# Performance work log

Measured on AMD Instinct MI355X. Metric: run time of the kernel, lower is better.

Reference implementation:

```python
import jax, jax.numpy as jnp
import numpy as np

BN_EPS = 1e-3
SLOPE = 0.1
K = 100
CLUSTER_TEMP = 5.0


def setup_inputs() -> dict:
    key = jax.random.key(0)
    ks = jax.random.split(key, 5)
    N, Cin, Cout = 8192, 1, 64
    d = 49 * Cout  # (28/4)^2 * out_channels
    return {
        "x": jax.random.normal(ks[0], (N, Cin, 28, 28), jnp.float32),
        "conv1_w": jax.random.normal(ks[1], (128, Cin, 5, 5), jnp.float32) * 0.05,
        "conv1_b": jnp.zeros((128,), jnp.float32),
        "bn1_gamma": jnp.ones((128,), jnp.float32),
        "bn1_beta": jnp.zeros((128,), jnp.float32),
        "bn1_mean": jnp.zeros((128,), jnp.float32),
        "bn1_var": jnp.ones((128,), jnp.float32),
        "conv2_w": jax.random.normal(ks[2], (Cout, 128, 5, 5), jnp.float32) * 0.02,
        "conv2_b": jnp.zeros((Cout,), jnp.float32),
        "bn2_gamma": jnp.ones((Cout,), jnp.float32),
        "bn2_beta": jnp.zeros((Cout,), jnp.float32),
        "bn2_mean": jnp.zeros((Cout,), jnp.float32),
        "bn2_var": jnp.ones((Cout,), jnp.float32),
        "init_mu": jax.random.uniform(ks[3], (K, d), jnp.float32),
        "num_iter": 10,
    }


def _conv_bn_lrelu(x, w, b, gamma, beta, mean, var):
    # Conv2d(k=5, s=2, p=2) -> BatchNorm (eval/running stats) -> LeakyReLU(0.1)
    h = jax.lax.conv_general_dilated(
        x, w, window_strides=(2, 2), padding=[(2, 2), (2, 2)],
        dimension_numbers=("NCHW", "OIHW", "NCHW"))
    h = h + b[None, :, None, None]
    inv = gamma * jax.lax.rsqrt(var + BN_EPS)
    h = h * inv[None, :, None, None] + (beta - mean * inv)[None, :, None, None]
    return jnp.where(h >= 0, h, SLOPE * h)


def _cluster(data, mu, num_iter):
    # Row L2-normalize (equivalent to diag(1/||row||) @ data)
    data = data / jnp.linalg.norm(data, axis=1, keepdims=True)  # [n, d]
    for _ in range(num_iter):
        dist = data @ mu.T                                 # [n, K]
        r = jax.nn.softmax(CLUSTER_TEMP * dist, axis=1)    # [n, K]
        cluster_r = r.sum(axis=0)                          # [K]
        cluster_mean = r.T @ data                          # [K, d]
        mu = cluster_mean / cluster_r[:, None]
    dist = data @ mu.T
    r = jax.nn.softmax(CLUSTER_TEMP * dist, axis=1)
    return mu, r, dist


def reference(x, conv1_w, conv1_b, bn1_gamma, bn1_beta, bn1_mean, bn1_var,
              conv2_w, conv2_b, bn2_gamma, bn2_beta, bn2_mean, bn2_var,
              init_mu, num_iter):
    h = _conv_bn_lrelu(x, conv1_w, conv1_b, bn1_gamma, bn1_beta, bn1_mean, bn1_var)
    h = _conv_bn_lrelu(h, conv2_w, conv2_b, bn2_gamma, bn2_beta, bn2_mean, bn2_var)
    embeds = h.reshape(h.shape[0], -1)                     # [N, 49*Cout]
    mu_init, _, _ = _cluster(embeds, init_mu, int(num_iter))
    mu, r, dist = _cluster(embeds, jax.lax.stop_gradient(mu_init), 1)
    return mu, r, dist
```

## Files before the change

kernel.cpp:

```cpp
#include <hip/hip_runtime.h>
#include <hip/hip_bf16.h>
#include <math.h>

#define BN_EPS 1e-3f
#define SLOPE  0.1f
#define TEMP   5.0f
#define DDIM   3136

typedef __attribute__((ext_vector_type(8))) short bf16x8;
typedef __attribute__((ext_vector_type(4))) float f32x4;

static __device__ __forceinline__ short f2b(float f) {
  __hip_bfloat16 h = __float2bfloat16(f);
  return *reinterpret_cast<short*>(&h);
}

#define W2B_OFF   0u
#define W1B_OFF   102400u
#define DB_OFF    204800u
#define DB_SZ     (8192u*3136u/2u)
#define DT_OFF    (DB_OFF + DB_SZ)
#define DT_SZ     (8192u*3136u/2u)
#define MUB_OFF   (DT_OFF + DT_SZ)
#define MUB_SZ    (112u*3136u/2u)
#define MUF_OFF   (MUB_OFF + MUB_SZ)
#define MUF_SZ    (100u*3136u)
#define CMS_OFF   (MUF_OFF + MUF_SZ)
#define CMS_SZ    (8u*3136u*112u)
#define RT_OFF    (CMS_OFF + CMS_SZ)
#define RT_SZ     (112u*8192u/2u)
#define CR_OFF    (RT_OFF + RT_SZ)

__global__ __launch_bounds__(256) void k_w2b(const float* __restrict__ w2,
                                             __hip_bfloat16* __restrict__ w2b) {
  int idx = blockIdx.x * 256 + threadIdx.x;
  if (idx >= 204800) return;
  int ci   = idx & 31;
  int lr   = (idx >> 5) & 15;
  int rest = idx >> 9;
  int kk   = rest % 100;
  int oct  = rest / 100;
  int oc   = oct * 16 + lr;
  int tap  = kk >> 2;
  int c    = ((kk & 3) << 5) + ci;
  w2b[idx] = __float2bfloat16(w2[(oc * 128 + c) * 25 + tap]);
}

__global__ __launch_bounds__(256) void k_w1b(const float* __restrict__ w1,
                                             __hip_bfloat16* __restrict__ w1b) {
  int idx = blockIdx.x * 256 + threadIdx.x;
  if (idx >= 4096) return;
  int k   = idx & 31;
  int lr  = (idx >> 5) & 15;
  int oct = idx >> 9;
  int oc  = oct * 16 + lr;
  float v = (k < 25) ? w1[oc * 25 + k] : 0.f;
  w1b[idx] = __float2bfloat16(v);
}

__global__ __launch_bounds__(256) void k_conv(
    const float* __restrict__ x,
    const __hip_bfloat16* __restrict__ w1bh, const float* __restrict__ b1,
    const float* __restrict__ g1,  const float* __restrict__ be1,
    const float* __restrict__ mn1, const float* __restrict__ vr1,
    const __hip_bfloat16* __restrict__ w2bh, const float* __restrict__ b2,
    const float* __restrict__ g2,  const float* __restrict__ be2,
    const float* __restrict__ mn2, const float* __restrict__ vr2,
    __hip_bfloat16* __restrict__ db) {
  __shared__ float xs[1024];
  __shared__ float bn2s[128];
  __shared__ float bn1a[128], bn1b[128];
  __shared__ float nrm[4];
  __shared__ __align__(16) __hip_bfloat16 h1s[197 * 128];

  const int t    = threadIdx.x;
  const int img  = blockIdx.x;
  const int lane = t & 63;
  const int wv   = t >> 6;
  const int lr   = lane & 15;
  const int kg   = lane >> 4;
  const short* w2b = (const short*)w2bh;
  const short* w1b = (const short*)w1bh;

  for (int i = t; i < 1024; i += 256) xs[i] = 0.f;
  if (t < 64) {
    float a2 = g2[t] * rsqrtf(vr2[t] + BN_EPS);
    bn2s[t]      = a2;
    bn2s[64 + t] = b2[t] * a2 + be2[t] - mn2[t] * a2;
    ((unsigned*)(h1s + 196 * 128))[t] = 0u;
  }
  if (t < 128) {
    float a1 = g1[t] * rsqrtf(vr1[t] + BN_EPS);
    bn1a[t] = a1;
    bn1b[t] = b1[t] * a1 + be1[t] - mn1[t] * a1;
  }
  __syncthreads();
  const float* xi = x + (size_t)img * 784;
  for (int i = t; i < 784; i += 256) {
    int yy = i / 28, xx = i % 28;
    xs[(yy + 2) * 32 + (xx + 2)] = xi[i];
  }
  __syncthreads();

  {
    bf16x8 a0 = *(const bf16x8*)(w1b + (2 * wv) * 512 + lr * 32 + kg * 8);
    bf16x8 a1 = *(const bf16x8*)(w1b + (2 * wv + 1) * 512 + lr * 32 + kg * 8);
    for (int pt = 0; pt < 13; ++pt) {
      const int px  = pt * 16 + lr;
      const int pxc = (px < 196) ? px : 195;
      const int oy  = pxc / 14, ox = pxc - 14 * (pxc / 14);
      const float* xb = xs + (2 * oy) * 32 + 2 * ox;
      short bs[8];
#pragma unroll
      for (int j = 0; j < 8; ++j) {
        int k   = kg * 8 + j;
        int tap = (k < 25) ? k : 0;
        int kh  = tap / 5, kw = tap - 5 * (tap / 5);
        bs[j] = f2b(xb[kh * 32 + kw]);
      }
      bf16x8 b;
#pragma unroll
      for (int j = 0; j < 8; ++j) b[j] = bs[j];
      f32x4 c0 = {0.f, 0.f, 0.f, 0.f}, c1 = {0.f, 0.f, 0.f, 0.f};
      c0 = __builtin_amdgcn_mfma_f32_16x16x32_bf16(a0, b, c0, 0, 0, 0);
      c1 = __builtin_amdgcn_mfma_f32_16x16x32_bf16(a1, b, c1, 0, 0, 0);
      if (px < 196) {
        const int swz = (px & 7) << 4;
        unsigned w0lo, w0hi, w1lo, w1hi;
        {
          float v[4], u[4];
#pragma unroll
          for (int r = 0; r < 4; ++r) {
            int oc = wv * 32 + kg * 4 + r;
            float h = c0[r] * bn1a[oc] + bn1b[oc];
            v[r] = (h >= 0.f) ? h : SLOPE * h;
            int oc2 = oc + 16;
            float h2 = c1[r] * bn1a[oc2] + bn1b[oc2];
            u[r] = (h2 >= 0.f) ? h2 : SLOPE * h2;
          }
          w0lo = (unsigned)(unsigned short)f2b(v[0]) |
                 ((unsigned)(unsigned short)f2b(v[1]) << 16);
          w0hi = (unsigned)(unsigned short)f2b(v[2]) |
                 ((unsigned)(unsigned short)f2b(v[3]) << 16);
          w1lo = (unsigned)(unsigned short)f2b(u[0]) |
                 ((unsigned)(unsigned short)f2b(u[1]) << 16);
          w1hi = (unsigned)(unsigned short)f2b(u[2]) |
                 ((unsigned)(unsigned short)f2b(u[3]) << 16);
        }
        char* base = (char*)h1s + px * 256;
        const int o0 = ((wv * 32 + kg * 4) * 2) ^ swz;
        const int o1 = ((wv * 32 + 16 + kg * 4) * 2) ^ swz;
        *(uint2*)(base + o0) = make_uint2(w0lo, w0hi);
        *(uint2*)(base + o1) = make_uint2(w1lo, w1hi);
      }
    }
  }
  __syncthreads();

  const int woff  = lr * 32 + kg * 8;
  const int kgoff = kg << 4;
  int pxA[4], oyA[4], oxA[4];
#pragma unroll
  for (int pt = 0; pt < 4; ++pt) {
    int p = pt * 16 + lr;
    pxA[pt] = p;
    oyA[pt] = p / 7;
    oxA[pt] = p - 7 * oyA[pt];
  }

  f32x4 acc[4][4];
#pragma unroll
  for (int oct = 0; oct < 4; ++oct)
#pragma unroll
    for (int pt = 0; pt < 4; ++pt) acc[oct][pt] = (f32x4){0.f, 0.f, 0.f, 0.f};

  const int s0 = 25 * wv, s1e = s0 + 25;
  int curtap = -1;
  int rowB[4], rowS[4];

  auto loadk = [&](int kk, bf16x8* areg, bf16x8* breg) {
    int tap = kk >> 2;
    if (tap != curtap) {
      curtap = tap;
      int kh = tap / 5, kw = tap - 5 * (tap / 5);
#pragma unroll
      for (int pt = 0; pt < 4; ++pt) {
        int iy = 2 * oyA[pt] - 2 + kh;
        int ix = 2 * oxA[pt] - 2 + kw;
        bool val = (pxA[pt] < 49) & ((unsigned)iy < 14u) & ((unsigned)ix < 14u);
        int ip = val ? iy * 14 + ix : 196;
        rowB[pt] = ip * 256;
        rowS[pt] = (ip & 7) << 4;
      }
    }
    int c01 = (kk & 3) << 6;
#pragma unroll
    for (int oct = 0; oct < 4; ++oct)
      areg[oct] = *(const bf16x8*)(w2b + ((oct * 100 + kk) << 9) + woff);
#pragma unroll
    for (int pt = 0; pt < 4; ++pt)
      breg[pt] = *(const bf16x8*)((const char*)h1s + rowB[pt] +
                                  ((c01 | kgoff) ^ rowS[pt]));
  };

  bf16x8 a[4], b[4], an[4], bn_[4];
  loadk(s0, a, b);
  for (int kk = s0; kk < s1e; ++kk) {
    if (kk + 1 < s1e) loadk(kk + 1, an, bn_);
#pragma unroll
    for (int oct = 0; oct < 4; ++oct)
#pragma unroll
      for (int pt = 0; pt < 4; ++pt)
        acc[oct][pt] = __builtin_amdgcn_mfma_f32_16x16x32_bf16(a[oct], b[pt],
                                                               acc[oct][pt], 0, 0, 0);
#pragma unroll
    for (int q = 0; q < 4; ++q) { a[q] = an[q]; b[q] = bn_[q]; }
  }
  __syncthreads();

  float* red = (float*)h1s;
  if (wv != 0) {
#pragma unroll
    for (int oct = 0; oct < 4; ++oct)
#pragma unroll
      for (int pt = 0; pt < 4; ++pt)
#pragma unroll
        for (int r = 0; r < 4; ++r)
          red[(wv - 1) * 4096 + ((oct * 4 + pt) * 4 + r) * 64 + lane] =
              acc[oct][pt][r];
  }
  __syncthreads();
  if (wv == 0) {
#pragma unroll
    for (int oct = 0; oct < 4; ++oct)
#pragma unroll
      for (int pt = 0; pt < 4; ++pt)
#pragma unroll
        for (int r = 0; r < 4; ++r) {
          const int i = (oct * 4 + pt) * 4 + r;
          float v = acc[oct][pt][r] + red[i * 64 + lane] +
                    red[4096 + i * 64 + lane] + red[8192 + i * 64 + lane];
          red[i * 64 + lane] = v;
        }
  }
  __syncthreads();

  float outv[16];
  float ss = 0.f;
#pragma unroll
  for (int pt = 0; pt < 4; ++pt) {
#pragma unroll
    for (int r = 0; r < 4; ++r) {
      const int i = ((wv * 4 + pt) * 4 + r);
      float v = red[i * 64 + lane];
      const int oc = wv * 16 + kg * 4 + r;
      v = v * bn2s[oc] + bn2s[64 + oc];
      v = (v >= 0.f) ? v : SLOPE * v;
      outv[pt * 4 + r] = v;
      if (pxA[pt] < 49) ss += v * v;
    }
  }
#pragma unroll
  for (int m = 1; m < 64; m <<= 1) ss += __shfl_xor(ss, m, 64);
  if (lane == 0) nrm[wv] = ss;
  __syncthreads();
  const float invn = rsqrtf(nrm[0] + nrm[1] + nrm[2] + nrm[3]);
  __hip_bfloat16* dro = db + (size_t)img * DDIM;
#pragma unroll
  for (int pt = 0; pt < 4; ++pt) {
    if (pxA[pt] < 49) {
#pragma unroll
      for (int r = 0; r < 4; ++r) {
        const int oc = wv * 16 + kg * 4 + r;
        dro[oc * 49 + pxA[pt]] = __float2bfloat16(outv[pt * 4 + r] * invn);
      }
    }
  }
}

__global__ __launch_bounds__(256) void k_tr(const __hip_bfloat16* __restrict__ dbh,
                                            __hip_bfloat16* __restrict__ dTh) {
  __shared__ short tile[64][72];
  const int t   = threadIdx.x;
  const int i   = t >> 2;
  const int seg = t & 3;
  const size_t img0 = (size_t)blockIdx.x * 64;
  const size_t d0   = (size_t)blockIdx.y * 64;
  const short* src = (const short*)dbh + (img0 + i) * DDIM + d0 + seg * 16;
  bf16x8 v0 = *(const bf16x8*)src;
  bf16x8 v1 = *(const bf16x8*)(src + 8);
  *(bf16x8*)&tile[i][seg * 16]     = v0;
  *(bf16x8*)&tile[i][seg * 16 + 8] = v1;
  __syncthreads();
  short tmp[16];
#pragma unroll
  for (int k = 0; k < 16; ++k) tmp[k] = tile[seg * 16 + k][i];
  short* dst = (short*)dTh + (d0 + i) * 8192 + img0 + seg * 16;
  *(bf16x8*)dst       = *(bf16x8*)tmp;
  *(bf16x8*)(dst + 8) = *((bf16x8*)tmp + 1);
}

__global__ __launch_bounds__(256) void k_muinit(const float* __restrict__ mu0,
                                                __hip_bfloat16* __restrict__ mub) {
  int idx = blockIdx.x * 256 + threadIdx.x;
  if (idx >= 112 * DDIM) return;
  int j = idx / DDIM, d = idx - j * DDIM;
  float v = (j < 100) ? mu0[j * DDIM + d] : 0.f;
  mub[idx] = __float2bfloat16(v);
}

__global__ __launch_bounds__(256) void k_dsm(
    const __hip_bfloat16* __restrict__ data,
    const __hip_bfloat16* __restrict__ mu,
    __hip_bfloat16* __restrict__ rT,
    float* __restrict__ cr,
    float* __restrict__ outr,
    float* __restrict__ outd,
    int final_flag) {
  __shared__ float red[3][64][28];
  const int t    = threadIdx.x;
  const int lane = t & 63;
  const int wv   = t >> 6;
  const int rowbase = blockIdx.x * 16;
  const int s0 = (98 * wv) >> 2;
  const int s1 = (98 * (wv + 1)) >> 2;
  const int lr = lane & 15;
  const int kg = lane >> 4;

  const __hip_bfloat16* arow = data + (size_t)(rowbase + lr) * DDIM + kg * 8;
  const __hip_bfloat16* brow = mu + (size_t)lr * DDIM + kg * 8;

  f32x4 acc[7];
#pragma unroll
  for (int i = 0; i < 7; ++i) acc[i] = (f32x4){0.f, 0.f, 0.f, 0.f};

  bf16x8 a, b[7], an, bn_[7];
  {
    const int k0 = s0 * 32;
    a = *(const bf16x8*)(arow + k0);
#pragma unroll
    for (int tl = 0; tl < 7; ++tl)
      b[tl] = *(const bf16x8*)(brow + (size_t)tl * 16 * DDIM + k0);
  }
  for (int s = s0; s < s1; ++s) {
    if (s + 1 < s1) {
      const int k1 = (s + 1) * 32;
      an = *(const bf16x8*)(arow + k1);
#pragma unroll
      for (int tl = 0; tl < 7; ++tl)
        bn_[tl] = *(const bf16x8*)(brow + (size_t)tl * 16 * DDIM + k1);
    }
#pragma unroll
    for (int tl = 0; tl < 7; ++tl)
      acc[tl] = __builtin_amdgcn_mfma_f32_16x16x32_bf16(a, b[tl], acc[tl], 0, 0, 0);
    a = an;
#pragma unroll
    for (int tl = 0; tl < 7; ++tl) b[tl] = bn_[tl];
  }

  if (wv != 0) {
#pragma unroll
    for (int tl = 0; tl < 7; ++tl)
#pragma unroll
      for (int r = 0; r < 4; ++r) red[wv - 1][lane][tl * 4 + r] = acc[tl][r];
  }
  __syncthreads();
  if (wv != 0) return;

#pragma unroll
  for (int tl = 0; tl < 7; ++tl)
#pragma unroll
    for (int r = 0; r < 4; ++r)
      acc[tl][r] += red[0][lane][tl * 4 + r] + red[1][lane][tl * 4 + r] +
                    red[2][lane][tl * 4 + r];

  if (final_flag) {
#pragma unroll
    for (int tl = 0; tl < 7; ++tl) {
      const int col = tl * 16 + lr;
      if (col < 100) {
#pragma unroll
        for (int r = 0; r < 4; ++r)
          outd[(size_t)(rowbase + kg * 4 + r) * 100 + col] = acc[tl][r];
      }
    }
  }

#pragma unroll
  for (int r = 0; r < 4; ++r) {
    float m = -1e30f;
#pragma unroll
    for (int tl = 0; tl < 7; ++tl) {
      const bool valid = (tl < 6) || (lr < 4);
      m = fmaxf(m, valid ? acc[tl][r] : -1e30f);
    }
    m = fmaxf(m, __shfl_xor(m, 1, 64));
    m = fmaxf(m, __shfl_xor(m, 2, 64));
    m = fmaxf(m, __shfl_xor(m, 4, 64));
    m = fmaxf(m, __shfl_xor(m, 8, 64));
    float s = 0.f;
    float e[7];
#pragma unroll
    for (int tl = 0; tl < 7; ++tl) {
      const bool valid = (tl < 6) || (lr < 4);
      e[tl] = valid ? __expf(TEMP * (acc[tl][r] - m)) : 0.f;
      s += e[tl];
    }
    s += __shfl_xor(s, 1, 64);
    s += __shfl_xor(s, 2, 64);
    s += __shfl_xor(s, 4, 64);
    s += __shfl_xor(s, 8, 64);
    const float inv = 1.f / s;
#pragma unroll
    for (int tl = 0; tl < 7; ++tl) acc[tl][r] = e[tl] * inv;
  }

  if (final_flag) {
#pragma unroll
    for (int tl = 0; tl < 7; ++tl) {
      const int col = tl * 16 + lr;
      if (col < 100) {
#pragma unroll
        for (int r = 0; r < 4; ++r)
          outr[(size_t)(rowbase + kg * 4 + r) * 100 + col] = acc[tl][r];
      }
    }
    return;
  }

#pragma unroll
  for (int tl = 0; tl < 7; ++tl) {
    const int col = tl * 16 + lr;
    if (col < 100) {
#pragma unroll
      for (int r = 0; r < 4; ++r)
        rT[(size_t)col * 8192 + rowbase + kg * 4 + r] = __float2bfloat16(acc[tl][r]);
    }
  }
  float csum[7];
#pragma unroll
  for (int tl = 0; tl < 7; ++tl) {
    float cs = acc[tl][0] + acc[tl][1] + acc[tl][2] + acc[tl][3];
    cs += __shfl_xor(cs, 16, 64);
    cs += __shfl_xor(cs, 32, 64);
    csum[tl] = cs;
  }
  if (lane < 16) {
#pragma unroll
    for (int tl = 0; tl < 7; ++tl) {
      const int col = tl * 16 + lane;
      if (col < 100) atomicAdd(cr + col, csum[tl]);
    }
  }
}

__global__ __launch_bounds__(256) void k_mu(
    const __hip_bfloat16* __restrict__ dataT,
    const __hip_bfloat16* __restrict__ rT,
    float* __restrict__ cms) {
  const int t    = threadIdx.x;
  const int lane = t & 63;
  const int wv   = t >> 6;
  const int mbase = blockIdx.x * 64 + wv * 16;
  const int kbase = blockIdx.y * 1024;
  const int lr = lane & 15;
  const int kg = lane >> 4;

  const __hip_bfloat16* arow = dataT + (size_t)(mbase + lr) * 8192 + kbase + kg * 8;
  const __hip_bfloat16* brow = rT + (size_t)lr * 8192 + kbase + kg * 8;

  f32x4 acc[7];
#pragma unroll
  for (int i = 0; i < 7; ++i) acc[i] = (f32x4){0.f, 0.f, 0.f, 0.f};

  bf16x8 a, b[7], an, bn_[7];
  a = *(const bf16x8*)(arow);
#pragma unroll
  for (int tl = 0; tl < 7; ++tl)
    b[tl] = *(const bf16x8*)(brow + (size_t)tl * 16 * 8192);
  for (int s = 0; s < 32; ++s) {
    if (s + 1 < 32) {
      const int k1 = (s + 1) * 32;
      an = *(const bf16x8*)(arow + k1);
#pragma unroll
      for (int tl = 0; tl < 7; ++tl)
        bn_[tl] = *(const bf16x8*)(brow + (size_t)tl * 16 * 8192 + k1);
    }
#pragma unroll
    for (int tl = 0; tl < 7; ++tl)
      acc[tl] = __builtin_amdgcn_mfma_f32_16x16x32_bf16(a, b[tl], acc[tl], 0, 0, 0);
    a = an;
#pragma unroll
    for (int tl = 0; tl < 7; ++tl) b[tl] = bn_[tl];
  }

  float* dst = cms + (size_t)blockIdx.y * (3136u * 112u);
#pragma unroll
  for (int tl = 0; tl < 7; ++tl) {
    const int col = tl * 16 + lr;
#pragma unroll
    for (int r = 0; r < 4; ++r)
      dst[(size_t)(mbase + kg * 4 + r) * 112 + col] = acc[tl][r];
  }
}

__global__ __launch_bounds__(256) void k_upd(const float* __restrict__ cms,
                                             const float* __restrict__ cr,
                                             float* __restrict__ muf,
                                             __hip_bfloat16* __restrict__ mub) {
  int idx = blockIdx.x * 256 + threadIdx.x;
  if (idx >= 100 * DDIM) return;
  int j = idx / DDIM, d = idx - j * DDIM;
  float v = 0.f;
#pragma unroll
  for (int s = 0; s < 8; ++s)
    v += cms[(size_t)s * (3136u * 112u) + (size_t)d * 112 + j];
  v /= cr[j];
  muf[idx] = v;
  mub[idx] = __float2bfloat16(v);
}

extern "C" void kernel_launch(void* const* d_in, const int* in_sizes, int n_in,
                              void* d_out, int out_size, void* d_ws, size_t ws_size,
                              hipStream_t stream) {
  const float* x   = (const float*)d_in[0];
  const float* w1  = (const float*)d_in[1];
  const float* b1  = (const float*)d_in[2];
  const float* g1  = (const float*)d_in[3];
  const float* be1 = (const float*)d_in[4];
  const float* mn1 = (const float*)d_in[5];
  const float* vr1 = (const float*)d_in[6];
  const float* w2  = (const float*)d_in[7];
  const float* b2  = (const float*)d_in[8];
  const float* g2  = (const float*)d_in[9];
  const float* be2 = (const float*)d_in[10];
  const float* mn2 = (const float*)d_in[11];
  const float* vr2 = (const float*)d_in[12];
  const float* mu0 = (const float*)d_in[13];

  float* ws = (float*)d_ws;
  __hip_bfloat16* w2b = (__hip_bfloat16*)(ws + W2B_OFF);
  __hip_bfloat16* w1b = (__hip_bfloat16*)(ws + W1B_OFF);
  __hip_bfloat16* db  = (__hip_bfloat16*)(ws + DB_OFF);
  __hip_bfloat16* dT  = (__hip_bfloat16*)(ws + DT_OFF);
  __hip_bfloat16* mub = (__hip_bfloat16*)(ws + MUB_OFF);
  float*          muf = ws + MUF_OFF;
  float*          cms = ws + CMS_OFF;
  __hip_bfloat16* rT  = (__hip_bfloat16*)(ws + RT_OFF);
  float*          cr  = ws + CR_OFF;
  float*          out = (float*)d_out;

  k_w2b<<<800, 256, 0, stream>>>(w2, w2b);
  k_w1b<<<16, 256, 0, stream>>>(w1, w1b);
  k_conv<<<8192, 256, 0, stream>>>(x, w1b, b1, g1, be1, mn1, vr1,
                                   w2b, b2, g2, be2, mn2, vr2, db);
  k_tr<<<dim3(128, 49), 256, 0, stream>>>(db, dT);
  k_muinit<<<(112 * DDIM + 255) / 256, 256, 0, stream>>>(mu0, mub);
  hipMemsetAsync(rT + (size_t)100 * 8192, 0, 12 * 8192 * sizeof(__hip_bfloat16),
                 stream);

  for (int it = 0; it < 11; ++it) {
    hipMemsetAsync(cr, 0, 128 * sizeof(float), stream);
    k_dsm<<<512, 256, 0, stream>>>(db, mub, rT, cr, nullptr, nullptr, 0);
    k_mu<<<dim3(49, 8), 256, 0, stream>>>(dT, rT, cms);
    k_upd<<<(100 * DDIM + 255) / 256, 256, 0, stream>>>(cms, cr, muf, mub);
  }

  k_dsm<<<512, 256, 0, stream>>>(db, mub, rT, cr, out + 313600, out + 1132800, 1);
  hipMemcpyAsync(out, muf, (size_t)MUF_SZ * sizeof(float),
                 hipMemcpyDeviceToDevice, stream);
}
```

Baseline: 1.891 ms.

## Widen split-K in distance and centroid GEMMs, bf16 partials, tiled update

The distance/softmax kernel now runs 8 waves per block, each covering one eighth of the K dimension, with a larger LDS reduction (padded to avoid bank conflicts). The centroid GEMM splits K into 16 slices instead of 8, giving more blocks for occupancy, and stores its partial sums as bf16 to halve write and read traffic. The update kernel is rewritten to stage the partials in a shared-memory tile so the transpose reads and writes coalesce. The bf16 partials lose precision in the accumulation, and the extra split-K adds reduction work.

After: 1.850 ms. -2.1%, faster.

```diff
diff --git a/kernel.cpp b/kernel.cpp
--- a/kernel.cpp
+++ b/kernel.cpp
@@ -26,7 +26,7 @@
 #define MUF_OFF   (MUB_OFF + MUB_SZ)
 #define MUF_SZ    (100u*3136u)
 #define CMS_OFF   (MUF_OFF + MUF_SZ)
-#define CMS_SZ    (8u*3136u*112u)
+#define CMS_SZ    (16u*3136u*112u/2u)
 #define RT_OFF    (CMS_OFF + CMS_SZ)
 #define RT_SZ     (112u*8192u/2u)
 #define CR_OFF    (RT_OFF + RT_SZ)
@@ -309,7 +309,7 @@
   mub[idx] = __float2bfloat16(v);
 }
 
-__global__ __launch_bounds__(256) void k_dsm(
+__global__ __launch_bounds__(512) void k_dsm(
     const __hip_bfloat16* __restrict__ data,
     const __hip_bfloat16* __restrict__ mu,
     __hip_bfloat16* __restrict__ rT,
@@ -317,13 +317,13 @@
     float* __restrict__ outr,
     float* __restrict__ outd,
     int final_flag) {
-  __shared__ float red[3][64][28];
+  __shared__ float red[7][64][29];
   const int t    = threadIdx.x;
   const int lane = t & 63;
   const int wv   = t >> 6;
   const int rowbase = blockIdx.x * 16;
-  const int s0 = (98 * wv) >> 2;
-  const int s1 = (98 * (wv + 1)) >> 2;
+  const int s0 = (98 * wv) >> 3;
+  const int s1 = (98 * (wv + 1)) >> 3;
   const int lr = lane & 15;
   const int kg = lane >> 4;
 
@@ -370,9 +370,12 @@
 #pragma unroll
   for (int tl = 0; tl < 7; ++tl)
 #pragma unroll
-    for (int r = 0; r < 4; ++r)
-      acc[tl][r] += red[0][lane][tl * 4 + r] + red[1][lane][tl * 4 + r] +
-                    red[2][lane][tl * 4 + r];
+    for (int r = 0; r < 4; ++r) {
+      float v = acc[tl][r];
+#pragma unroll
+      for (int bk = 0; bk < 7; ++bk) v += red[bk][lane][tl * 4 + r];
+      acc[tl][r] = v;
+    }
 
   if (final_flag) {
 #pragma unroll
@@ -457,12 +460,12 @@
 __global__ __launch_bounds__(256) void k_mu(
     const __hip_bfloat16* __restrict__ dataT,
     const __hip_bfloat16* __restrict__ rT,
-    float* __restrict__ cms) {
+    __hip_bfloat16* __restrict__ cms) {
   const int t    = threadIdx.x;
   const int lane = t & 63;
   const int wv   = t >> 6;
   const int mbase = blockIdx.x * 64 + wv * 16;
-  const int kbase = blockIdx.y * 1024;
+  const int kbase = blockIdx.y * 512;
   const int lr = lane & 15;
   const int kg = lane >> 4;
 
@@ -478,8 +481,8 @@
 #pragma unroll
   for (int tl = 0; tl < 7; ++tl)
     b[tl] = *(const bf16x8*)(brow + (size_t)tl * 16 * 8192);
-  for (int s = 0; s < 32; ++s) {
-    if (s + 1 < 32) {
+  for (int s = 0; s < 16; ++s) {
+    if (s + 1 < 16) {
       const int k1 = (s + 1) * 32;
       an = *(const bf16x8*)(arow + k1);
 #pragma unroll
@@ -494,30 +497,39 @@
     for (int tl = 0; tl < 7; ++tl) b[tl] = bn_[tl];
   }
 
-  float* dst = cms + (size_t)blockIdx.y * (3136u * 112u);
+  __hip_bfloat16* dst = cms + (size_t)blockIdx.y * (3136u * 112u);
 #pragma unroll
   for (int tl = 0; tl < 7; ++tl) {
     const int col = tl * 16 + lr;
 #pragma unroll
     for (int r = 0; r < 4; ++r)
-      dst[(size_t)(mbase + kg * 4 + r) * 112 + col] = acc[tl][r];
-  }
-}
-
-__global__ __launch_bounds__(256) void k_upd(const float* __restrict__ cms,
+      dst[(size_t)(mbase + kg * 4 + r) * 112 + col] = __float2bfloat16(acc[tl][r]);
+  }
+}
+
+__global__ __launch_bounds__(256) void k_upd(const __hip_bfloat16* __restrict__ cms,
                                              const float* __restrict__ cr,
                                              float* __restrict__ muf,
                                              __hip_bfloat16* __restrict__ mub) {
-  int idx = blockIdx.x * 256 + threadIdx.x;
-  if (idx >= 100 * DDIM) return;
-  int j = idx / DDIM, d = idx - j * DDIM;
-  float v = 0.f;
-#pragma unroll
-  for (int s = 0; s < 8; ++s)
-    v += cms[(size_t)s * (3136u * 112u) + (size_t)d * 112 + j];
-  v /= cr[j];
-  muf[idx] = v;
-  mub[idx] = __float2bfloat16(v);
+  __shared__ float tile[64][113];
+  const int t  = threadIdx.x;
+  const int d0 = blockIdx.x * 64;
+  for (int e = t; e < 64 * 112; e += 256) {
+    int dd = e / 112, jj = e - dd * 112;
+    const __hip_bfloat16* p = cms + (size_t)(d0 + dd) * 112 + jj;
+    float v = 0.f;
+#pragma unroll
+    for (int s2 = 0; s2 < 16; ++s2)
+      v += __bfloat162float(p[(size_t)s2 * (3136u * 112u)]);
+    tile[dd][jj] = v;
+  }
+  __syncthreads();
+  for (int e = t; e < 100 * 64; e += 256) {
+    int jj = e >> 6, dd = e & 63;
+    float v = tile[dd][jj] / cr[jj];
+    muf[(size_t)jj * DDIM + d0 + dd] = v;
+    mub[(size_t)jj * DDIM + d0 + dd] = __float2bfloat16(v);
+  }
 }
 
 extern "C" void kernel_launch(void* const* d_in, const int* in_sizes, int n_in,
@@ -545,7 +557,7 @@
   __hip_bfloat16* dT  = (__hip_bfloat16*)(ws + DT_OFF);
   __hip_bfloat16* mub = (__hip_bfloat16*)(ws + MUB_OFF);
   float*          muf = ws + MUF_OFF;
-  float*          cms = ws + CMS_OFF;
+  __hip_bfloat16* cms = (__hip_bfloat16*)(ws + CMS_OFF);
   __hip_bfloat16* rT  = (__hip_bfloat16*)(ws + RT_OFF);
   float*          cr  = ws + CR_OFF;
   float*          out = (float*)d_out;
@@ -561,12 +573,12 @@
 
   for (int it = 0; it < 11; ++it) {
     hipMemsetAsync(cr, 0, 128 * sizeof(float), stream);
-    k_dsm<<<512, 256, 0, stream>>>(db, mub, rT, cr, nullptr, nullptr, 0);
-    k_mu<<<dim3(49, 8), 256, 0, stream>>>(dT, rT, cms);
-    k_upd<<<(100 * DDIM + 255) / 256, 256, 0, stream>>>(cms, cr, muf, mub);
-  }
-
-  k_dsm<<<512, 256, 0, stream>>>(db, mub, rT, cr, out + 313600, out + 1132800, 1);
+    k_dsm<<<512, 512, 0, stream>>>(db, mub, rT, cr, nullptr, nullptr, 0);
+    k_mu<<<dim3(49, 16), 256, 0, stream>>>(dT, rT, cms);
+    k_upd<<<49, 256, 0, stream>>>(cms, cr, muf, mub);
+  }
+
+  k_dsm<<<512, 512, 0, stream>>>(db, mub, rT, cr, out + 313600, out + 1132800, 1);
   hipMemcpyAsync(out, muf, (size_t)MUF_SZ * sizeof(float),
                  hipMemcpyDeviceToDevice, stream);
 }
```
